# Kernel optimization log

Hardware: AMD Instinct MI355X
Metric: run time of the kernel (lower is better)

The kernel has to match this reference:

```python
import jax, jax.numpy as jnp
import numpy as np

NEG_SLOPE = 0.01  # F.leaky_relu default
NUM_GRAPHS = 64


def sage_conv(x, src, dst, W_l, b_l, W_r):
    """PyG SAGEConv (mean aggr): lin_l(mean_j x_j) + lin_r(x_i)."""
    n = x.shape[0]
    msg = x[src]                                               # [E, C] gather
    agg = jax.ops.segment_sum(msg, dst, num_segments=n)        # [N, C] scatter-add
    deg = jax.ops.segment_sum(jnp.ones_like(dst, dtype=x.dtype), dst, num_segments=n)
    mean = agg / jnp.maximum(deg, 1.0)[:, None]
    return mean @ W_l + b_l + x @ W_r


def setup_inputs() -> dict:
    key = jax.random.key(0)
    ks = jax.random.split(key, 12)
    N, E, C, H, O = 50000, 600000, 128, 128, 2
    x = jax.random.normal(ks[0], (N, C), dtype=jnp.float32)
    edge_index = jax.random.randint(ks[1], (2, E), 0, N, dtype=jnp.int64)
    batch = jnp.sort(jax.random.randint(ks[2], (N,), 0, NUM_GRAPHS, dtype=jnp.int64))

    def lin(k, fin, fout):
        return jax.random.normal(k, (fin, fout), dtype=jnp.float32) / np.sqrt(fin)

    return {
        "x": x, "edge_index": edge_index, "batch": batch,
        "W1_l": lin(ks[3], C, H), "b1": jnp.zeros((H,), jnp.float32), "W1_r": lin(ks[4], C, H),
        "W2_l": lin(ks[5], H, H), "b2": jnp.zeros((H,), jnp.float32), "W2_r": lin(ks[6], H, H),
        "W3_l": lin(ks[7], H, H), "b3": jnp.zeros((H,), jnp.float32), "W3_r": lin(ks[8], H, H),
        "W_fc": lin(ks[9], H, O), "b_fc": jnp.zeros((O,), jnp.float32),
    }


def reference(x, edge_index, batch, W1_l, b1, W1_r, W2_l, b2, W2_r,
              W3_l, b3, W3_r, W_fc, b_fc):
    src, dst = edge_index[0], edge_index[1]
    h = jax.nn.leaky_relu(sage_conv(x, src, dst, W1_l, b1, W1_r), NEG_SLOPE)
    h = jax.nn.leaky_relu(sage_conv(h, src, dst, W2_l, b2, W2_r), NEG_SLOPE)
    h = jax.nn.leaky_relu(sage_conv(h, src, dst, W3_l, b3, W3_r), NEG_SLOPE)
    pooled = jax.ops.segment_max(h, batch, num_segments=NUM_GRAPHS)  # global_max_pool
    return pooled @ W_fc + b_fc
```

## Files before the change

kernel.cpp:

```cpp
#include <hip/hip_runtime.h>
#include <hip/hip_bf16.h>

#define NEG_SLOPE 0.01f
#define C 128
#define NGRAPH 64
#define CAP 64

typedef short short8 __attribute__((ext_vector_type(8)));
typedef float f32x4 __attribute__((ext_vector_type(4)));
typedef unsigned short ushort;

__device__ __forceinline__ unsigned fmap(float x){
  unsigned b = __float_as_uint(x);
  return (b & 0x80000000u) ? ~b : (b | 0x80000000u);
}
__device__ __forceinline__ float funmap(unsigned k){
  return (k & 0x80000000u) ? __uint_as_float(k & 0x7FFFFFFFu) : __uint_as_float(~k);
}

__device__ __forceinline__ ushort bf16_rne(float a){
  unsigned u = __float_as_uint(a);
  return (ushort)((u + 0x7FFFu + ((u >> 16) & 1u)) >> 16);
}
__device__ __forceinline__ float b2f(ushort h){
  return __uint_as_float(((unsigned)h) << 16);
}

__device__ __forceinline__ void lds_dma16(const void* g, void* l){
  __builtin_amdgcn_global_load_lds(
      (const __attribute__((address_space(1))) unsigned int*)(void*)g,
      (__attribute__((address_space(3))) unsigned int*)(void*)l, 16, 0, 0);
}

__global__ void prep_kernel(const float* __restrict__ x, ushort* __restrict__ xb, int nx4,
                            const int* __restrict__ src, const int* __restrict__ dst,
                            int* __restrict__ cursor, ushort* __restrict__ csr, int E,
                            const float* __restrict__ W1l, const float* __restrict__ W1r,
                            const float* __restrict__ W2l, const float* __restrict__ W2r,
                            const float* __restrict__ W3l, const float* __restrict__ W3r,
                            short* __restrict__ B1, short* __restrict__ B2,
                            short* __restrict__ B3,
                            int nblk_x, int nblk_e){
  int bid = blockIdx.x;
  if(bid < nblk_e){
    int e = bid * 256 + threadIdx.x;
    if(e < E){
      int d = dst[e];
      int p = atomicAdd(&cursor[d], 1);
      if(p < CAP) csr[(long long)d * CAP + p] = (ushort)src[e];
    }
    return;
  }
  bid -= nblk_e;
  if(bid < nblk_x){
    int i = (bid * 256 + threadIdx.x) * 4;
    if(i < nx4){
      float4 v = *(const float4*)(x + i);
      ushort4 r = make_ushort4(bf16_rne(v.x), bf16_rne(v.y), bf16_rne(v.z), bf16_rne(v.w));
      *(ushort4*)(xb + i) = r;
    }
    return;
  }
  bid -= nblk_x;
  int set = bid >> 7;
  int idx = (bid & 127) * 256 + threadIdx.x;
  const float* Wl = (set == 0) ? W1l : (set == 1) ? W2l : W3l;
  const float* Wr = (set == 0) ? W1r : (set == 1) ? W2r : W3r;
  short* Bpk      = (set == 0) ? B1  : (set == 1) ? B2  : B3;
  int k = idx >> 7, n = idx & 127;
  float w = (k < C) ? Wl[k * C + n] : Wr[(k - C) * C + n];
  ushort hi = bf16_rne(w);
  float r = w - b2f(hi);
  ushort lo = bf16_rne(r);
  int kstep = k >> 5, kg = (k >> 3) & 3, j = k & 7;
  int pos = ((kstep * 4 + kg) * C + n) * 8 + j;
  Bpk[pos] = (short)hi;
  Bpk[pos + 32768] = (short)lo;
}

__global__ __launch_bounds__(256, 2) void layer_fused(
    const ushort* __restrict__ xin, const ushort* __restrict__ csr,
    const int* __restrict__ cnt, const short* __restrict__ Bpk,
    const float* __restrict__ bias,
    ushort* __restrict__ Hout, int M,
    const int* __restrict__ batch, unsigned* __restrict__ pooled)
{
  __shared__ ushort Ms[64 * 136];
  __shared__ __align__(16) ushort Xs[64 * 32];
  int tid = threadIdx.x;
  int bm = blockIdx.x * 64;
  int lane = tid & 63;
  int wn = tid >> 6;
  int lg = lane >> 4;
  int lm = lane & 15;

  {
    int grp = tid >> 4, g15 = tid & 15, gbase = tid & 48;
    float a[4][8];
#pragma unroll
    for(int k = 0; k < 4; k++)
#pragma unroll
      for(int f = 0; f < 8; f++) a[k][f] = 0.f;
    int dg[4];
    const ushort* ep[4];
#pragma unroll
    for(int k = 0; k < 4; k++){
      int node = bm + grp + k * 16;
      if(node < M){
        int d = cnt[node];
        dg[k] = d < CAP ? d : CAP;
        ep[k] = csr + (long long)node * CAP;
      }else{
        dg[k] = 0;
        ep[k] = csr;
      }
    }
    int maxd = dg[0];
    maxd = dg[1] > maxd ? dg[1] : maxd;
    maxd = dg[2] > maxd ? dg[2] : maxd;
    maxd = dg[3] > maxd ? dg[3] : maxd;

    for(int base = 0; base < maxd; base += 16){
      int ids[4];
#pragma unroll
      for(int k = 0; k < 4; k++)
        ids[k] = (base + g15 < dg[k]) ? (int)ep[k][base + g15] : 0;
      int lim = maxd - base; if(lim > 16) lim = 16;
      for(int j = 0; j < lim; j += 2){
        short8 r[4][2];
#pragma unroll
        for(int k = 0; k < 4; k++){
#pragma unroll
          for(int u = 0; u < 2; u++){
            int s = __shfl(ids[k], gbase + j + u, 64);
            r[k][u] = *(const short8*)(xin + (long long)s * C + g15 * 8);
          }
        }
#pragma unroll
        for(int k = 0; k < 4; k++){
#pragma unroll
          for(int u = 0; u < 2; u++){
            if(base + j + u < dg[k]){
#pragma unroll
              for(int f = 0; f < 8; f++) a[k][f] += b2f((ushort)r[k][u][f]);
            }
          }
        }
      }
    }
#pragma unroll
    for(int k = 0; k < 4; k++){
      float sc = 1.0f / fmaxf((float)dg[k], 1.0f);
      short8 o;
#pragma unroll
      for(int f = 0; f < 8; f++) o[f] = (short)bf16_rne(a[k][f] * sc);
      *(short8*)(Ms + (grp + k * 16) * 136 + g15 * 8) = o;
    }
  }

  int srow = tid >> 2;
  int sslice = (tid & 3) ^ ((tid >> 3) & 3);
  int grow = bm + srow; if(grow >= M) grow = M - 1;
  const long long goff = (long long)grow * C + sslice * 8;
  ushort* ldsbase = Xs + wn * 512;

  f32x4 acc[4][2];
#pragma unroll
  for(int i = 0; i < 4; i++)
#pragma unroll
    for(int j = 0; j < 2; j++)
      acc[i][j] = (f32x4){0.f, 0.f, 0.f, 0.f};

  short8 bh[2][2], bl[2][2];
  auto loadB = [&](int ks, int buf){
#pragma unroll
    for(int j = 0; j < 2; j++){
      const short* bp = Bpk + (((ks * 4 + lg) * C) + wn * 32 + j * 16 + lm) * 8;
      bh[buf][j] = *(const short8*)bp;
      bl[buf][j] = *(const short8*)(bp + 32768);
    }
  };
  loadB(0, 0);
  __syncthreads();

#pragma unroll
  for(int ks = 0; ks < 8; ks++){
    if(ks >= 4){
      if(ks > 4) __syncthreads();
      lds_dma16(xin + goff + (ks - 4) * 32, ldsbase);
    }
    if(ks < 7) loadB(ks + 1, (ks + 1) & 1);
    if(ks >= 4) __syncthreads();

    short8 af[4];
    if(ks < 4){
#pragma unroll
      for(int i = 0; i < 4; i++)
        af[i] = *(const short8*)(Ms + (i * 16 + lm) * 136 + ks * 32 + lg * 8);
    }else{
#pragma unroll
      for(int i = 0; i < 4; i++){
        int r = i * 16 + lm;
        int slot = lg ^ ((r >> 1) & 3);
        af[i] = *(const short8*)(Xs + r * 32 + slot * 8);
      }
    }
    int b = ks & 1;
#pragma unroll
    for(int i = 0; i < 4; i++)
#pragma unroll
      for(int j = 0; j < 2; j++){
        acc[i][j] = __builtin_amdgcn_mfma_f32_16x16x32_bf16(af[i], bh[b][j], acc[i][j], 0, 0, 0);
        acc[i][j] = __builtin_amdgcn_mfma_f32_16x16x32_bf16(af[i], bl[b][j], acc[i][j], 0, 0, 0);
      }
  }

  if(pooled == nullptr){
#pragma unroll
    for(int j = 0; j < 2; j++){
      int col = wn * 32 + j * 16 + lm;
      float bv = bias[col];
#pragma unroll
      for(int i = 0; i < 4; i++){
#pragma unroll
        for(int reg = 0; reg < 4; reg++){
          int row = bm + i * 16 + lg * 4 + reg;
          if(row < M){
            float v = acc[i][j][reg] + bv;
            v = v > 0.f ? v : NEG_SLOPE * v;
            Hout[(long long)row * C + col] = bf16_rne(v);
          }
        }
      }
    }
  }else{
#pragma unroll
    for(int i = 0; i < 4; i++){
      int row0 = bm + i * 16 + lg * 4;
      if(row0 >= M) continue;
      bool whole = (row0 + 3 < M);
      int g0 = batch[row0];
      bool same = whole && (batch[row0 + 3] == g0);
#pragma unroll
      for(int j = 0; j < 2; j++){
        int col = wn * 32 + j * 16 + lm;
        float bv = bias[col];
        float v0 = acc[i][j][0] + bv; v0 = v0 > 0.f ? v0 : NEG_SLOPE * v0;
        float v1 = acc[i][j][1] + bv; v1 = v1 > 0.f ? v1 : NEG_SLOPE * v1;
        float v2 = acc[i][j][2] + bv; v2 = v2 > 0.f ? v2 : NEG_SLOPE * v2;
        float v3 = acc[i][j][3] + bv; v3 = v3 > 0.f ? v3 : NEG_SLOPE * v3;
        if(same){
          float m01 = fmaxf(v0, v1), m23 = fmaxf(v2, v3);
          atomicMax(&pooled[g0 * C + col], fmap(fmaxf(m01, m23)));
        }else{
          float vv[4] = {v0, v1, v2, v3};
#pragma unroll
          for(int reg = 0; reg < 4; reg++){
            int row = row0 + reg;
            if(row < M) atomicMax(&pooled[batch[row] * C + col], fmap(vv[reg]));
          }
        }
      }
    }
  }
}

__global__ void fc_kernel(const unsigned* __restrict__ pooled_u, const float* __restrict__ Wfc,
                          const float* __restrict__ bfc, float* __restrict__ out){
  int t = threadIdx.x;
  int g = t >> 1, o = t & 1;
  float s = bfc[o];
  for(int k = 0; k < C; k++)
    s += funmap(pooled_u[g * C + k]) * Wfc[k * 2 + o];
  out[g * 2 + o] = s;
}

extern "C" void kernel_launch(void* const* d_in, const int* in_sizes, int n_in,
                              void* d_out, int out_size, void* d_ws, size_t ws_size,
                              hipStream_t stream) {
  const float* x    = (const float*)d_in[0];
  const int*   ei   = (const int*)d_in[1];
  const int*   batch= (const int*)d_in[2];
  const float* W1l  = (const float*)d_in[3];
  const float* b1   = (const float*)d_in[4];
  const float* W1r  = (const float*)d_in[5];
  const float* W2l  = (const float*)d_in[6];
  const float* b2   = (const float*)d_in[7];
  const float* W2r  = (const float*)d_in[8];
  const float* W3l  = (const float*)d_in[9];
  const float* b3   = (const float*)d_in[10];
  const float* W3r  = (const float*)d_in[11];
  const float* Wfc  = (const float*)d_in[12];
  const float* bfc  = (const float*)d_in[13];
  float* out = (float*)d_out;

  const int N = in_sizes[0] / C;
  const int E = in_sizes[1] / 2;
  const int* srcv = ei;
  const int* dstv = ei + E;

  char* ws = (char*)d_ws;
  size_t off = 0;
  auto alloc = [&](size_t bytes) -> void* {
    void* p = ws + off;
    off += (bytes + 255) & ~(size_t)255;
    return p;
  };
  int*      cursor = (int*)alloc((size_t)N * 4);
  unsigned* pooled = (unsigned*)alloc((size_t)NGRAPH * C * 4);
  size_t    zbytes = off;
  ushort*   csr    = (ushort*)alloc((size_t)N * CAP * 2);
  ushort*   xb     = (ushort*)alloc((size_t)N * C * 2);
  ushort*   h1b    = (ushort*)alloc((size_t)N * C * 2);
  short*    B1     = (short*)alloc((size_t)2 * 2 * C * C * 2);
  short*    B2     = (short*)alloc((size_t)2 * 2 * C * C * 2);
  short*    B3     = (short*)alloc((size_t)2 * 2 * C * C * 2);

  hipMemsetAsync(cursor, 0, zbytes, stream);

  const int nbx  = (N * C / 4 + 255) / 256;
  const int nbe  = (E + 255) / 256;
  const int nbp  = 3 * 128;
  prep_kernel<<<nbe + nbx + nbp, 256, 0, stream>>>(
      x, xb, N * C, srcv, dstv, cursor, csr, E,
      W1l, W1r, W2l, W2r, W3l, W3r, B1, B2, B3, nbx, nbe);

  int lblocks = (N + 63) / 64;

  layer_fused<<<lblocks, 256, 0, stream>>>(xb, csr, cursor, B1, b1,
                                           h1b, N, nullptr, nullptr);
  layer_fused<<<lblocks, 256, 0, stream>>>(h1b, csr, cursor, B2, b2,
                                           xb, N, nullptr, nullptr);
  layer_fused<<<lblocks, 256, 0, stream>>>(xb, csr, cursor, B3, b3,
                                           nullptr, N, batch, pooled);

  fc_kernel<<<1, 128, 0, stream>>>(pooled, Wfc, bfc, out);
}
```

Before: 262.7 us.

## Use 512-thread blocks, split columns across 8 waves, preload root features once

Doubles the threads per 64-node block to 512 (8 waves). Each thread now gathers neighbours for 2 nodes instead of 4, four neighbours per step. In the GEMM each wave owns 16 output columns instead of 32. All four K-slices of the root-feature tile are DMA'd into a larger LDS buffer once, before the K loop, which removes the per-step barriers of the old streamed loads. The aim is more memory-level parallelism in the gather and fewer synchronisations, at the cost of more LDS per block and a higher occupancy target that may limit registers.

```diff
diff --git a/kernel.cpp b/kernel.cpp
--- a/kernel.cpp
+++ b/kernel.cpp
@@ -78,7 +78,7 @@
   Bpk[pos + 32768] = (short)lo;
 }
 
-__global__ __launch_bounds__(256, 2) void layer_fused(
+__global__ __launch_bounds__(512, 4) void layer_fused(
     const ushort* __restrict__ xin, const ushort* __restrict__ csr,
     const int* __restrict__ cnt, const short* __restrict__ Bpk,
     const float* __restrict__ bias,
@@ -86,7 +86,7 @@
     const int* __restrict__ batch, unsigned* __restrict__ pooled)
 {
   __shared__ ushort Ms[64 * 136];
-  __shared__ __align__(16) ushort Xs[64 * 32];
+  __shared__ __align__(16) ushort Xs4[4 * 2048];
   int tid = threadIdx.x;
   int bm = blockIdx.x * 64;
   int lane = tid & 63;
@@ -96,16 +96,16 @@
 
   {
     int grp = tid >> 4, g15 = tid & 15, gbase = tid & 48;
-    float a[4][8];
-#pragma unroll
-    for(int k = 0; k < 4; k++)
+    float a[2][8];
+#pragma unroll
+    for(int k = 0; k < 2; k++)
 #pragma unroll
       for(int f = 0; f < 8; f++) a[k][f] = 0.f;
-    int dg[4];
-    const ushort* ep[4];
-#pragma unroll
-    for(int k = 0; k < 4; k++){
-      int node = bm + grp + k * 16;
+    int dg[2];
+    const ushort* ep[2];
+#pragma unroll
+    for(int k = 0; k < 2; k++){
+      int node = bm + grp + k * 32;
       if(node < M){
         int d = cnt[node];
         dg[k] = d < CAP ? d : CAP;
@@ -115,31 +115,28 @@
         ep[k] = csr;
       }
     }
-    int maxd = dg[0];
-    maxd = dg[1] > maxd ? dg[1] : maxd;
-    maxd = dg[2] > maxd ? dg[2] : maxd;
-    maxd = dg[3] > maxd ? dg[3] : maxd;
+    int maxd = dg[0] > dg[1] ? dg[0] : dg[1];
 
     for(int base = 0; base < maxd; base += 16){
-      int ids[4];
-#pragma unroll
-      for(int k = 0; k < 4; k++)
+      int ids[2];
+#pragma unroll
+      for(int k = 0; k < 2; k++)
         ids[k] = (base + g15 < dg[k]) ? (int)ep[k][base + g15] : 0;
       int lim = maxd - base; if(lim > 16) lim = 16;
-      for(int j = 0; j < lim; j += 2){
-        short8 r[4][2];
-#pragma unroll
-        for(int k = 0; k < 4; k++){
-#pragma unroll
-          for(int u = 0; u < 2; u++){
+      for(int j = 0; j < lim; j += 4){
+        short8 r[2][4];
+#pragma unroll
+        for(int k = 0; k < 2; k++){
+#pragma unroll
+          for(int u = 0; u < 4; u++){
             int s = __shfl(ids[k], gbase + j + u, 64);
             r[k][u] = *(const short8*)(xin + (long long)s * C + g15 * 8);
           }
         }
 #pragma unroll
-        for(int k = 0; k < 4; k++){
-#pragma unroll
-          for(int u = 0; u < 2; u++){
+        for(int k = 0; k < 2; k++){
+#pragma unroll
+          for(int u = 0; u < 4; u++){
             if(base + j + u < dg[k]){
 #pragma unroll
               for(int f = 0; f < 8; f++) a[k][f] += b2f((ushort)r[k][u][f]);
@@ -149,48 +146,43 @@
       }
     }
 #pragma unroll
-    for(int k = 0; k < 4; k++){
+    for(int k = 0; k < 2; k++){
       float sc = 1.0f / fmaxf((float)dg[k], 1.0f);
       short8 o;
 #pragma unroll
       for(int f = 0; f < 8; f++) o[f] = (short)bf16_rne(a[k][f] * sc);
-      *(short8*)(Ms + (grp + k * 16) * 136 + g15 * 8) = o;
-    }
-  }
-
-  int srow = tid >> 2;
-  int sslice = (tid & 3) ^ ((tid >> 3) & 3);
-  int grow = bm + srow; if(grow >= M) grow = M - 1;
-  const long long goff = (long long)grow * C + sslice * 8;
-  ushort* ldsbase = Xs + wn * 512;
-
-  f32x4 acc[4][2];
+      *(short8*)(Ms + (grp + k * 32) * 136 + g15 * 8) = o;
+    }
+  }
+
+  f32x4 acc[4];
 #pragma unroll
   for(int i = 0; i < 4; i++)
-#pragma unroll
-    for(int j = 0; j < 2; j++)
-      acc[i][j] = (f32x4){0.f, 0.f, 0.f, 0.f};
-
-  short8 bh[2][2], bl[2][2];
+    acc[i] = (f32x4){0.f, 0.f, 0.f, 0.f};
+
+  short8 bh[2], bl[2];
   auto loadB = [&](int ks, int buf){
-#pragma unroll
-    for(int j = 0; j < 2; j++){
-      const short* bp = Bpk + (((ks * 4 + lg) * C) + wn * 32 + j * 16 + lm) * 8;
-      bh[buf][j] = *(const short8*)bp;
-      bl[buf][j] = *(const short8*)(bp + 32768);
-    }
+    const short* bp = Bpk + (((ks * 4 + lg) * C) + wn * 16 + lm) * 8;
+    bh[buf] = *(const short8*)bp;
+    bl[buf] = *(const short8*)(bp + 32768);
   };
   loadB(0, 0);
   __syncthreads();
 
 #pragma unroll
+  for(int t = 0; t < 2; t++){
+    int u = wn + t * 8;
+    int s = u >> 2, q = u & 3;
+    int rg = q * 16 + (lane >> 2);
+    int gs = (lane & 3) ^ ((rg >> 1) & 3);
+    int growx = bm + rg; if(growx >= M) growx = M - 1;
+    lds_dma16(xin + (long long)growx * C + s * 32 + gs * 8, Xs4 + u * 512);
+  }
+
+#pragma unroll
   for(int ks = 0; ks < 8; ks++){
-    if(ks >= 4){
-      if(ks > 4) __syncthreads();
-      lds_dma16(xin + goff + (ks - 4) * 32, ldsbase);
-    }
+    if(ks == 4) __syncthreads();
     if(ks < 7) loadB(ks + 1, (ks + 1) & 1);
-    if(ks >= 4) __syncthreads();
 
     short8 af[4];
     if(ks < 4){
@@ -202,34 +194,29 @@
       for(int i = 0; i < 4; i++){
         int r = i * 16 + lm;
         int slot = lg ^ ((r >> 1) & 3);
-        af[i] = *(const short8*)(Xs + r * 32 + slot * 8);
+        af[i] = *(const short8*)(Xs4 + (ks - 4) * 2048 + r * 32 + slot * 8);
       }
     }
     int b = ks & 1;
 #pragma unroll
-    for(int i = 0; i < 4; i++)
-#pragma unroll
-      for(int j = 0; j < 2; j++){
-        acc[i][j] = __builtin_amdgcn_mfma_f32_16x16x32_bf16(af[i], bh[b][j], acc[i][j], 0, 0, 0);
-        acc[i][j] = __builtin_amdgcn_mfma_f32_16x16x32_bf16(af[i], bl[b][j], acc[i][j], 0, 0, 0);
-      }
-  }
-
+    for(int i = 0; i < 4; i++){
+      acc[i] = __builtin_amdgcn_mfma_f32_16x16x32_bf16(af[i], bh[b], acc[i], 0, 0, 0);
+      acc[i] = __builtin_amdgcn_mfma_f32_16x16x32_bf16(af[i], bl[b], acc[i], 0, 0, 0);
+    }
+  }
+
+  int col = wn * 16 + lm;
+  float bv = bias[col];
   if(pooled == nullptr){
 #pragma unroll
-    for(int j = 0; j < 2; j++){
-      int col = wn * 32 + j * 16 + lm;
-      float bv = bias[col];
-#pragma unroll
-      for(int i = 0; i < 4; i++){
-#pragma unroll
-        for(int reg = 0; reg < 4; reg++){
-          int row = bm + i * 16 + lg * 4 + reg;
-          if(row < M){
-            float v = acc[i][j][reg] + bv;
-            v = v > 0.f ? v : NEG_SLOPE * v;
-            Hout[(long long)row * C + col] = bf16_rne(v);
-          }
+    for(int i = 0; i < 4; i++){
+#pragma unroll
+      for(int reg = 0; reg < 4; reg++){
+        int row = bm + i * 16 + lg * 4 + reg;
+        if(row < M){
+          float v = acc[i][reg] + bv;
+          v = v > 0.f ? v : NEG_SLOPE * v;
+          Hout[(long long)row * C + col] = bf16_rne(v);
         }
       }
     }
@@ -241,24 +228,19 @@
       bool whole = (row0 + 3 < M);
       int g0 = batch[row0];
       bool same = whole && (batch[row0 + 3] == g0);
-#pragma unroll
-      for(int j = 0; j < 2; j++){
-        int col = wn * 32 + j * 16 + lm;
-        float bv = bias[col];
-        float v0 = acc[i][j][0] + bv; v0 = v0 > 0.f ? v0 : NEG_SLOPE * v0;
-        float v1 = acc[i][j][1] + bv; v1 = v1 > 0.f ? v1 : NEG_SLOPE * v1;
-        float v2 = acc[i][j][2] + bv; v2 = v2 > 0.f ? v2 : NEG_SLOPE * v2;
-        float v3 = acc[i][j][3] + bv; v3 = v3 > 0.f ? v3 : NEG_SLOPE * v3;
-        if(same){
-          float m01 = fmaxf(v0, v1), m23 = fmaxf(v2, v3);
-          atomicMax(&pooled[g0 * C + col], fmap(fmaxf(m01, m23)));
-        }else{
-          float vv[4] = {v0, v1, v2, v3};
-#pragma unroll
-          for(int reg = 0; reg < 4; reg++){
-            int row = row0 + reg;
-            if(row < M) atomicMax(&pooled[batch[row] * C + col], fmap(vv[reg]));
-          }
+      float v0 = acc[i][0] + bv; v0 = v0 > 0.f ? v0 : NEG_SLOPE * v0;
+      float v1 = acc[i][1] + bv; v1 = v1 > 0.f ? v1 : NEG_SLOPE * v1;
+      float v2 = acc[i][2] + bv; v2 = v2 > 0.f ? v2 : NEG_SLOPE * v2;
+      float v3 = acc[i][3] + bv; v3 = v3 > 0.f ? v3 : NEG_SLOPE * v3;
+      if(same){
+        float m01 = fmaxf(v0, v1), m23 = fmaxf(v2, v3);
+        atomicMax(&pooled[g0 * C + col], fmap(fmaxf(m01, m23)));
+      }else{
+        float vv[4] = {v0, v1, v2, v3};
+#pragma unroll
+        for(int reg = 0; reg < 4; reg++){
+          int row = row0 + reg;
+          if(row < M) atomicMax(&pooled[batch[row] * C + col], fmap(vv[reg]));
         }
       }
     }
@@ -327,11 +309,11 @@
 
   int lblocks = (N + 63) / 64;
 
-  layer_fused<<<lblocks, 256, 0, stream>>>(xb, csr, cursor, B1, b1,
+  layer_fused<<<lblocks, 512, 0, stream>>>(xb, csr, cursor, B1, b1,
                                            h1b, N, nullptr, nullptr);
-  layer_fused<<<lblocks, 256, 0, stream>>>(h1b, csr, cursor, B2, b2,
+  layer_fused<<<lblocks, 512, 0, stream>>>(h1b, csr, cursor, B2, b2,
                                            xb, N, nullptr, nullptr);
-  layer_fused<<<lblocks, 256, 0, stream>>>(xb, csr, cursor, B3, b3,
+  layer_fused<<<lblocks, 512, 0, stream>>>(xb, csr, cursor, B3, b3,
                                            nullptr, N, batch, pooled);
 
   fc_kernel<<<1, 128, 0, stream>>>(pooled, Wfc, bfc, out);
```

Measured after the change: 264.6 us. Within noise of the previous version (+0.7%).

## Split fused gather+GEMM layer into separate gather-mean and GEMM kernels

Applied to the files above, without the earlier changes.

Each SAGE layer's fused kernel is split in two. One kernel gathers neighbours and writes the mean aggregation to a new bf16 buffer in global memory, using 32 nodes per block and 4 rows in flight per step. A second GEMM kernel DMA-loads both the mean and self features into a 32KB LDS tile up front and runs the MFMA loop without per-step barriers, with a higher occupancy hint. This aims to improve occupancy and latency hiding in each phase, at the cost of an extra global write and read of the N×C mean tensor plus more kernel launches.

```diff
diff --git a/kernel.cpp b/kernel.cpp
--- a/kernel.cpp
+++ b/kernel.cpp
@@ -78,15 +78,80 @@
   Bpk[pos + 32768] = (short)lo;
 }
 
-__global__ __launch_bounds__(256, 2) void layer_fused(
-    const ushort* __restrict__ xin, const ushort* __restrict__ csr,
-    const int* __restrict__ cnt, const short* __restrict__ Bpk,
-    const float* __restrict__ bias,
+__global__ void gather_mean(const ushort* __restrict__ xin, const ushort* __restrict__ csr,
+                            const int* __restrict__ cnt, ushort* __restrict__ meanb, int M){
+  int tid = threadIdx.x;
+  int bm = blockIdx.x * 32;
+  int grp = tid >> 4, g15 = tid & 15, gbase = tid & 48;
+  float a[2][8];
+#pragma unroll
+  for(int k = 0; k < 2; k++)
+#pragma unroll
+    for(int f = 0; f < 8; f++) a[k][f] = 0.f;
+  int dg[2];
+  const ushort* ep[2];
+#pragma unroll
+  for(int k = 0; k < 2; k++){
+    int node = bm + grp + k * 16;
+    if(node < M){
+      int d = cnt[node];
+      dg[k] = d < CAP ? d : CAP;
+      ep[k] = csr + (long long)node * CAP;
+    }else{
+      dg[k] = 0;
+      ep[k] = csr;
+    }
+  }
+  int maxd = dg[0] > dg[1] ? dg[0] : dg[1];
+
+  for(int base = 0; base < maxd; base += 16){
+    int ids[2];
+#pragma unroll
+    for(int k = 0; k < 2; k++)
+      ids[k] = (base + g15 < dg[k]) ? (int)ep[k][base + g15] : 0;
+    int lim = maxd - base; if(lim > 16) lim = 16;
+    for(int j = 0; j < lim; j += 4){
+      short8 r[2][4];
+#pragma unroll
+      for(int k = 0; k < 2; k++){
+#pragma unroll
+        for(int u = 0; u < 4; u++){
+          int s = __shfl(ids[k], gbase + j + u, 64);
+          r[k][u] = *(const short8*)(xin + (long long)s * C + g15 * 8);
+        }
+      }
+#pragma unroll
+      for(int k = 0; k < 2; k++){
+#pragma unroll
+        for(int u = 0; u < 4; u++){
+          if(base + j + u < dg[k]){
+#pragma unroll
+            for(int f = 0; f < 8; f++) a[k][f] += b2f((ushort)r[k][u][f]);
+          }
+        }
+      }
+    }
+  }
+#pragma unroll
+  for(int k = 0; k < 2; k++){
+    int node = bm + grp + k * 16;
+    if(node < M){
+      float sc = 1.0f / fmaxf((float)dg[k], 1.0f);
+      short8 o;
+#pragma unroll
+      for(int f = 0; f < 8; f++) o[f] = (short)bf16_rne(a[k][f] * sc);
+      *(short8*)(meanb + (long long)node * C + g15 * 8) = o;
+    }
+  }
+}
+
+__global__ __launch_bounds__(256, 4) void sage_gemm(
+    const ushort* __restrict__ xin, const ushort* __restrict__ meanb,
+    const short* __restrict__ Bpk, const float* __restrict__ bias,
     ushort* __restrict__ Hout, int M,
     const int* __restrict__ batch, unsigned* __restrict__ pooled)
 {
-  __shared__ ushort Ms[64 * 136];
-  __shared__ __align__(16) ushort Xs[64 * 32];
+  __shared__ __align__(16) ushort Xs[8 * 2048];
   int tid = threadIdx.x;
   int bm = blockIdx.x * 64;
   int lane = tid & 63;
@@ -95,74 +160,19 @@
   int lm = lane & 15;
 
   {
-    int grp = tid >> 4, g15 = tid & 15, gbase = tid & 48;
-    float a[4][8];
-#pragma unroll
-    for(int k = 0; k < 4; k++)
-#pragma unroll
-      for(int f = 0; f < 8; f++) a[k][f] = 0.f;
-    int dg[4];
-    const ushort* ep[4];
-#pragma unroll
-    for(int k = 0; k < 4; k++){
-      int node = bm + grp + k * 16;
-      if(node < M){
-        int d = cnt[node];
-        dg[k] = d < CAP ? d : CAP;
-        ep[k] = csr + (long long)node * CAP;
-      }else{
-        dg[k] = 0;
-        ep[k] = csr;
-      }
-    }
-    int maxd = dg[0];
-    maxd = dg[1] > maxd ? dg[1] : maxd;
-    maxd = dg[2] > maxd ? dg[2] : maxd;
-    maxd = dg[3] > maxd ? dg[3] : maxd;
-
-    for(int base = 0; base < maxd; base += 16){
-      int ids[4];
-#pragma unroll
-      for(int k = 0; k < 4; k++)
-        ids[k] = (base + g15 < dg[k]) ? (int)ep[k][base + g15] : 0;
-      int lim = maxd - base; if(lim > 16) lim = 16;
-      for(int j = 0; j < lim; j += 2){
-        short8 r[4][2];
-#pragma unroll
-        for(int k = 0; k < 4; k++){
-#pragma unroll
-          for(int u = 0; u < 2; u++){
-            int s = __shfl(ids[k], gbase + j + u, 64);
-            r[k][u] = *(const short8*)(xin + (long long)s * C + g15 * 8);
-          }
-        }
-#pragma unroll
-        for(int k = 0; k < 4; k++){
-#pragma unroll
-          for(int u = 0; u < 2; u++){
-            if(base + j + u < dg[k]){
-#pragma unroll
-              for(int f = 0; f < 8; f++) a[k][f] += b2f((ushort)r[k][u][f]);
-            }
-          }
-        }
-      }
-    }
-#pragma unroll
-    for(int k = 0; k < 4; k++){
-      float sc = 1.0f / fmaxf((float)dg[k], 1.0f);
-      short8 o;
-#pragma unroll
-      for(int f = 0; f < 8; f++) o[f] = (short)bf16_rne(a[k][f] * sc);
-      *(short8*)(Ms + (grp + k * 16) * 136 + g15 * 8) = o;
-    }
-  }
-
-  int srow = tid >> 2;
-  int sslice = (tid & 3) ^ ((tid >> 3) & 3);
-  int grow = bm + srow; if(grow >= M) grow = M - 1;
-  const long long goff = (long long)grow * C + sslice * 8;
-  ushort* ldsbase = Xs + wn * 512;
+    int rq = lane >> 2, ls = lane & 3;
+#pragma unroll
+    for(int t = 0; t < 8; t++){
+      int u = t * 4 + wn;
+      int q = u & 3;
+      int sl = (u >> 2) & 3;
+      const ushort* srcp = (u < 16) ? meanb : xin;
+      int rg = q * 16 + rq;
+      int gs = ls ^ ((rg >> 1) & 3);
+      int grow = bm + rg; if(grow >= M) grow = M - 1;
+      lds_dma16(srcp + (long long)grow * C + sl * 32 + gs * 8, Xs + u * 512);
+    }
+  }
 
   f32x4 acc[4][2];
 #pragma unroll
@@ -185,25 +195,13 @@
 
 #pragma unroll
   for(int ks = 0; ks < 8; ks++){
-    if(ks >= 4){
-      if(ks > 4) __syncthreads();
-      lds_dma16(xin + goff + (ks - 4) * 32, ldsbase);
-    }
     if(ks < 7) loadB(ks + 1, (ks + 1) & 1);
-    if(ks >= 4) __syncthreads();
-
     short8 af[4];
-    if(ks < 4){
-#pragma unroll
-      for(int i = 0; i < 4; i++)
-        af[i] = *(const short8*)(Ms + (i * 16 + lm) * 136 + ks * 32 + lg * 8);
-    }else{
-#pragma unroll
-      for(int i = 0; i < 4; i++){
-        int r = i * 16 + lm;
-        int slot = lg ^ ((r >> 1) & 3);
-        af[i] = *(const short8*)(Xs + r * 32 + slot * 8);
-      }
+#pragma unroll
+    for(int i = 0; i < 4; i++){
+      int r = i * 16 + lm;
+      int slot = lg ^ ((r >> 1) & 3);
+      af[i] = *(const short8*)(Xs + ks * 2048 + r * 32 + slot * 8);
     }
     int b = ks & 1;
 #pragma unroll
@@ -312,6 +310,7 @@
   ushort*   csr    = (ushort*)alloc((size_t)N * CAP * 2);
   ushort*   xb     = (ushort*)alloc((size_t)N * C * 2);
   ushort*   h1b    = (ushort*)alloc((size_t)N * C * 2);
+  ushort*   meanb  = (ushort*)alloc((size_t)N * C * 2);
   short*    B1     = (short*)alloc((size_t)2 * 2 * C * C * 2);
   short*    B2     = (short*)alloc((size_t)2 * 2 * C * C * 2);
   short*    B3     = (short*)alloc((size_t)2 * 2 * C * C * 2);
@@ -325,14 +324,15 @@
       x, xb, N * C, srcv, dstv, cursor, csr, E,
       W1l, W1r, W2l, W2r, W3l, W3r, B1, B2, B3, nbx, nbe);
 
-  int lblocks = (N + 63) / 64;
-
-  layer_fused<<<lblocks, 256, 0, stream>>>(xb, csr, cursor, B1, b1,
-                                           h1b, N, nullptr, nullptr);
-  layer_fused<<<lblocks, 256, 0, stream>>>(h1b, csr, cursor, B2, b2,
-                                           xb, N, nullptr, nullptr);
-  layer_fused<<<lblocks, 256, 0, stream>>>(xb, csr, cursor, B3, b3,
-                                           nullptr, N, batch, pooled);
+  int gblocks = (N + 31) / 32;
+  int mblocks = (N + 63) / 64;
+
+  gather_mean<<<gblocks, 256, 0, stream>>>(xb, csr, cursor, meanb, N);
+  sage_gemm<<<mblocks, 256, 0, stream>>>(xb, meanb, B1, b1, h1b, N, nullptr, nullptr);
+  gather_mean<<<gblocks, 256, 0, stream>>>(h1b, csr, cursor, meanb, N);
+  sage_gemm<<<mblocks, 256, 0, stream>>>(h1b, meanb, B2, b2, xb, N, nullptr, nullptr);
+  gather_mean<<<gblocks, 256, 0, stream>>>(xb, csr, cursor, meanb, N);
+  sage_gemm<<<mblocks, 256, 0, stream>>>(xb, meanb, B3, b3, nullptr, N, batch, pooled);
 
   fc_kernel<<<1, 128, 0, stream>>>(pooled, Wfc, bfc, out);
 }
```

After: 265.8 us. Within noise of the previous version (+1.2%).

## Partition CSR build by destination range, predicate gathers, vectorize fc loads

Applied to the files above, without the earlier changes.

The edge scatter now runs as 16 destination partitions times 64 edge chunks. Each block re-reads its chunk of dst but only inserts edges whose destination falls in its partition, which keeps the atomic and CSR writes localized to a node range for better L2 and cache locality. In exchange, dst is read 16 times. The aggregation loop now marks padding neighbours with -1 and skips their loads with zero fill, replacing the per-element degree check. The fc kernel uses vectorized uint4/float4 loads.

```diff
diff --git a/kernel.cpp b/kernel.cpp
--- a/kernel.cpp
+++ b/kernel.cpp
@@ -5,6 +5,8 @@
 #define C 128
 #define NGRAPH 64
 #define CAP 64
+#define NPART 16
+#define NCHUNK 64
 
 typedef short short8 __attribute__((ext_vector_type(8)));
 typedef float f32x4 __attribute__((ext_vector_type(4)));
@@ -34,7 +36,7 @@
 
 __global__ void prep_kernel(const float* __restrict__ x, ushort* __restrict__ xb, int nx4,
                             const int* __restrict__ src, const int* __restrict__ dst,
-                            int* __restrict__ cursor, ushort* __restrict__ csr, int E,
+                            int* __restrict__ cursor, ushort* __restrict__ csr, int E, int N,
                             const float* __restrict__ W1l, const float* __restrict__ W1r,
                             const float* __restrict__ W2l, const float* __restrict__ W2r,
                             const float* __restrict__ W3l, const float* __restrict__ W3r,
@@ -43,11 +45,18 @@
                             int nblk_x, int nblk_e){
   int bid = blockIdx.x;
   if(bid < nblk_e){
-    int e = bid * 256 + threadIdx.x;
-    if(e < E){
+    int part  = bid & (NPART - 1);
+    int chunk = bid >> 4;
+    int lo = part * N / NPART, hi = (part + 1) * N / NPART;
+    int clen  = (E + NCHUNK - 1) / NCHUNK;
+    int ebase = chunk * clen;
+    int eend  = ebase + clen; if(eend > E) eend = E;
+    for(int e = ebase + threadIdx.x; e < eend; e += 256){
       int d = dst[e];
-      int p = atomicAdd(&cursor[d], 1);
-      if(p < CAP) csr[(long long)d * CAP + p] = (ushort)src[e];
+      if(d >= lo && d < hi){
+        int p = atomicAdd(&cursor[d], 1);
+        if(p < CAP) csr[(long long)d * CAP + p] = (ushort)src[e];
+      }
     }
     return;
   }
@@ -124,7 +133,7 @@
       int ids[4];
 #pragma unroll
       for(int k = 0; k < 4; k++)
-        ids[k] = (base + g15 < dg[k]) ? (int)ep[k][base + g15] : 0;
+        ids[k] = (base + g15 < dg[k]) ? (int)ep[k][base + g15] : -1;
       int lim = maxd - base; if(lim > 16) lim = 16;
       for(int j = 0; j < lim; j += 2){
         short8 r[4][2];
@@ -133,17 +142,17 @@
 #pragma unroll
           for(int u = 0; u < 2; u++){
             int s = __shfl(ids[k], gbase + j + u, 64);
-            r[k][u] = *(const short8*)(xin + (long long)s * C + g15 * 8);
+            short8 rv = {0, 0, 0, 0, 0, 0, 0, 0};
+            if(s >= 0) rv = *(const short8*)(xin + (long long)s * C + g15 * 8);
+            r[k][u] = rv;
           }
         }
 #pragma unroll
         for(int k = 0; k < 4; k++){
 #pragma unroll
           for(int u = 0; u < 2; u++){
-            if(base + j + u < dg[k]){
-#pragma unroll
-              for(int f = 0; f < 8; f++) a[k][f] += b2f((ushort)r[k][u][f]);
-            }
+#pragma unroll
+            for(int f = 0; f < 8; f++) a[k][f] += b2f((ushort)r[k][u][f]);
           }
         }
       }
@@ -270,8 +279,18 @@
   int t = threadIdx.x;
   int g = t >> 1, o = t & 1;
   float s = bfc[o];
-  for(int k = 0; k < C; k++)
-    s += funmap(pooled_u[g * C + k]) * Wfc[k * 2 + o];
+  const unsigned* pu = pooled_u + g * C;
+#pragma unroll
+  for(int k0 = 0; k0 < C; k0 += 4){
+    uint4 pv = *(const uint4*)(pu + k0);
+    float4 w0 = *(const float4*)(Wfc + k0 * 2);
+    float4 w1 = *(const float4*)(Wfc + k0 * 2 + 4);
+    float wa = o ? w0.y : w0.x;
+    float wb = o ? w0.w : w0.z;
+    float wc = o ? w1.y : w1.x;
+    float wd = o ? w1.w : w1.z;
+    s += funmap(pv.x) * wa + funmap(pv.y) * wb + funmap(pv.z) * wc + funmap(pv.w) * wd;
+  }
   out[g * 2 + o] = s;
 }
 
@@ -318,11 +337,11 @@
 
   hipMemsetAsync(cursor, 0, zbytes, stream);
 
+  const int nbe  = NPART * NCHUNK;
   const int nbx  = (N * C / 4 + 255) / 256;
-  const int nbe  = (E + 255) / 256;
   const int nbp  = 3 * 128;
   prep_kernel<<<nbe + nbx + nbp, 256, 0, stream>>>(
-      x, xb, N * C, srcv, dstv, cursor, csr, E,
+      x, xb, N * C, srcv, dstv, cursor, csr, E, N,
       W1l, W1r, W2l, W2r, W3l, W3r, B1, B2, B3, nbx, nbe);
 
   int lblocks = (N + 63) / 64;
```

Result: no change. 267.9 us (+2.0%).
